# Optimization experiments

Hardware: AMD Instinct MI355X
Metric: run time of the kernel (lower is better)

Reference implementation:

```python
import jax, jax.numpy as jnp
import numpy as np

L_IN, L_FREQ, L_OUT = 128, 64, 64
C_IN, C_OUT, T_DIM = 64, 64, 256
SPIN = 1

# ---------- self-contained spin-weighted SHT (MW sampling), replacing s2fft ----------

def _mw_thetas(L, extended):
    n = 2 * L - 1 if extended else L
    return (2 * np.arange(n) + 1) * np.pi / (2 * L - 1)

def _wigner_d_stack(L, thetas, n):
    # d^l_{m,n}(theta) = <l,m| exp(-i theta Jy) |l,n>, computed via eigh of the
    # Hermitian angular-momentum operator Jy. Output (ntheta, L, 2L-1), m at col L-1+m.
    nth = len(thetas)
    out = np.zeros((nth, L, 2 * L - 1), dtype=np.float64)
    for l in range(abs(n), L):
        dim = 2 * l + 1
        m = np.arange(-l, l).astype(np.float64)
        ap = np.sqrt(l * (l + 1.0) - m * (m + 1.0))
        Jy = np.zeros((dim, dim), dtype=np.complex128)
        i = np.arange(dim - 1)
        Jy[i + 1, i] = -0.5j * ap
        Jy[i, i + 1] = 0.5j * ap
        lam, V = np.linalg.eigh(Jy)
        coeff = V * np.conj(V[l + n, :])[None, :]
        phases = np.exp(-1j * np.outer(lam, thetas))
        out[:, l, L - 1 - l:L + l] = (coeff @ phases).T.real
    return out

def _mw_quad_weights(L):
    # per-theta weights on the mirror-extended grid: q_t = (1/(2L-1)) sum_k w(k) e^{ik theta_t}
    # with w(k) = int_0^pi e^{ik t} sin(t) dt
    k = np.arange(-(L - 1), L)
    den = np.where(np.abs(k) == 1, 1, 1 - k * k).astype(np.float64)
    w = np.where(k % 2 == 0, 2.0 / den, 0.0).astype(np.complex128)
    w[k == 1] = 0.5j * np.pi
    w[k == -1] = -0.5j * np.pi
    th = _mw_thetas(L, True)
    return ((w[None, :] * np.exp(1j * np.outer(th, k))).sum(1) / (2 * L - 1)).real

# transform kernels are constants (built once at import, numpy)
_D_FWD = jnp.asarray(_wigner_d_stack(L_IN, _mw_thetas(L_IN, True), -SPIN) * _mw_quad_weights(L_IN)[:, None, None], jnp.float32)
_D_INV = jnp.asarray(_wigner_d_stack(L_OUT, _mw_thetas(L_OUT, False), -SPIN), jnp.float32)
_CL_IN = jnp.asarray(((-1.0) ** SPIN) * np.sqrt((2 * np.arange(L_IN) + 1) / (4 * np.pi)), jnp.float32)
_CL_OUT = jnp.asarray(((-1.0) ** SPIN) * np.sqrt((2 * np.arange(L_OUT) + 1) / (4 * np.pi)), jnp.float32)
_m_all = np.arange(-(L_IN - 1), L_IN)
_PARITY = jnp.asarray(np.where((_m_all + SPIN) % 2 == 0, 1.0, -1.0), jnp.float32)

def sht_forward(x):
    # x: (L_IN, 2*L_IN-1, C) real spatial -> flm: (L_IN, 2*L_IN-1, C) complex, m at L_IN-1+m
    nphi = 2 * L_IN - 1
    ftm = jnp.fft.fftshift(jnp.fft.fft(x, axis=1), axes=1) * (2 * jnp.pi / nphi)
    # mirror extension in theta with (-1)^(m+spin) parity (all channels at once)
    g_ext = jnp.concatenate([ftm, _PARITY[None, :, None] * ftm[::-1][1:]], axis=0)
    flm = jnp.einsum('tlm,tmc->lmc', _D_FWD, g_ext)
    return flm * _CL_IN[:, None, None]

def sht_inverse(flm):
    # flm: (L_OUT, 2*L_OUT-1, C) complex -> (L_OUT, 2*L_OUT-1, C) real spatial
    ftm = jnp.einsum('tlm,lmc->tmc', _D_INV, flm * _CL_OUT[:, None, None])
    return (jnp.fft.ifft(jnp.fft.ifftshift(ftm, axes=1), axis=1) * (2 * L_OUT - 1)).real

def resize_flm(flm, l_in, l_out):
    # centered truncation / zero-pad of (L, 2L-1, C) harmonic coefficients
    if l_out <= l_in:
        d = l_in - l_out
        return flm[:l_out, d:d + 2 * l_out - 1]
    d = l_out - l_in
    return jnp.pad(flm, ((0, d), (d, d), (0, 0)))

# ---------- inputs and parameters ----------

def setup_inputs():
    key = jax.random.key(0)
    ks = jax.random.split(key, 12)
    n = lambda i, shape, s: jax.random.normal(ks[i], shape, jnp.float32) * s
    return {
        'x': jax.random.normal(ks[0], (L_IN, 2 * L_IN - 1, C_IN), jnp.float32),
        't_emb': jax.random.normal(ks[1], (T_DIM,), jnp.float32),
        'spec_conv_w': n(2, (C_IN, C_OUT), (1.0 / C_IN) ** 0.5),
        'spec_conv_b': jnp.zeros((C_OUT,), jnp.float32),
        'spec_wr': n(3, (L_FREQ, C_IN, C_OUT), (0.5 / C_IN) ** 0.5),
        'spec_wi': n(4, (L_FREQ, C_IN, C_OUT), (0.5 / C_IN) ** 0.5),
        'spec_tr_w': n(5, (T_DIM, L_FREQ), (1.0 / T_DIM) ** 0.5),
        'spec_tr_b': jnp.zeros((L_FREQ,), jnp.float32),
        'spec_ti_w': n(6, (T_DIM, L_FREQ), (1.0 / T_DIM) ** 0.5),
        'spec_ti_b': jnp.zeros((L_FREQ,), jnp.float32),
        'spat_conv1_w': n(7, (C_IN, C_OUT), (1.0 / C_IN) ** 0.5),
        'spat_conv1_b': jnp.zeros((C_OUT,), jnp.float32),
        'spat_t_w': n(8, (T_DIM, 2 * C_OUT), (1.0 / T_DIM) ** 0.5),
        'spat_t_b': jnp.zeros((2 * C_OUT,), jnp.float32),
        'spat_weight': n(9, (C_OUT, C_OUT), 0.01),
        'spat_conv2_w': n(10, (C_OUT, C_OUT), (1.0 / C_OUT) ** 0.5),
        'spat_conv2_b': jnp.zeros((C_OUT,), jnp.float32),
        'ln_scale': jnp.ones((C_OUT,), jnp.float32),
        'ln_bias': jnp.zeros((C_OUT,), jnp.float32),
    }

def reference(x, t_emb, spec_conv_w, spec_conv_b, spec_wr, spec_wi, spec_tr_w, spec_tr_b, spec_ti_w, spec_ti_b, spat_conv1_w, spat_conv1_b, spat_t_w, spat_t_b, spat_weight, spat_conv2_w, spat_conv2_b, ln_scale, ln_bias):
    # ----- SphericalSpectralTimeConv branch -----
    flm = sht_forward(x)                                   # (L_IN, 2L_IN-1, C_IN) complex
    flm = resize_flm(flm, L_IN, L_FREQ)                    # (L_FREQ, 2L_FREQ-1, C_IN)
    conv_flm = jnp.einsum('lmi,io->lmo', flm, spec_conv_w) + spec_conv_b
    t_c = (t_emb @ spec_tr_w + spec_tr_b) + 1j * (t_emb @ spec_ti_w + spec_ti_b)   # (L_FREQ,)
    w = t_c[:, None, None] * (spec_wr + 1j * spec_wi)      # (L_FREQ, C_IN, C_OUT)
    flm = jnp.einsum('lmi,lio->lmo', flm, w) + conv_flm
    xs = sht_inverse(resize_flm(flm, L_FREQ, L_OUT))       # (L_OUT, 2L_OUT-1, C_OUT) real
    xs = xs / (jnp.linalg.norm(xs, axis=-1, keepdims=True) + 1e-6)
    # ----- SpatialTimeConv branch (path='down') -----
    h = jnp.einsum('lmi,io->lmo', x, spat_conv1_w) + spat_conv1_b
    t = t_emb @ spat_t_w + spat_t_b
    w_t, b_t = t[:C_OUT], t[C_OUT:]
    h = jnp.einsum('lmi,io->lmo', h, w_t[None, :] * spat_weight)
    h = sht_inverse(resize_flm(sht_forward(h), L_IN, L_OUT))
    h = jnp.einsum('lmi,io->lmo', h, spat_conv2_w) + spat_conv2_b + b_t
    # ----- combine: add, gelu, LayerNorm (eps=1e-6 over channels) -----
    y = jax.nn.gelu(xs + h)
    mu = jnp.mean(y, axis=-1, keepdims=True)
    var = jnp.var(y, axis=-1, keepdims=True)
    return (y - mu) * jax.lax.rsqrt(var + 1e-6) * ln_scale + ln_bias
```

## Files before the change

### kernel.cpp

```cpp
#include <hip/hip_runtime.h>
#include <math.h>

#define DPI 3.141592653589793238462643383279502884

__device__ __forceinline__ float wave_sum64(float v) {
#pragma unroll
  for (int off = 32; off > 0; off >>= 1) v += __shfl_xor(v, off, 64);
  return v;
}

__device__ __forceinline__ float gelu_tanh(float v) {
  float u = 0.7978845608028654f * (v + 0.044715f * v * v * v);
  return 0.5f * v * (1.0f + tanhf(u));
}

#define CN255F ((float)(-2.0 * DPI / 255.0))
#define CN127F ((float)(2.0 * DPI / 127.0))


__device__ __forceinline__ void dft_block(int idx, int tid, const float* __restrict__ x,
                                          float* __restrict__ Are, float* __restrict__ Aim,
                                          float* __restrict__ Bre, float* __restrict__ Bim,
                                          char* sm) {
  float* xs_ = (float*)sm;
  int t = idx >> 2, ph = (idx >> 1) & 1, mh = idx & 1;
  float* ore = ph ? Bre : Are;
  float* oim = ph ? Bim : Aim;
  int pbase = ph * 128;
  int Ktot = ph ? 127 : 128;
  int cg_ = tid & 15, mg = tid >> 4;
  float wr[2], wi[2], rc[2], rs[2];
#pragma unroll
  for (int j = 0; j < 2; ++j) {
    int m = mh * 32 + mg * 2 + j;
    __sincosf(CN255F * (float)m, &rs[j], &rc[j]);
    int r0 = (m * pbase) % 255;
    __sincosf(CN255F * (float)r0, &wi[j], &wr[j]);
  }
  float accr[2][4], acci[2][4];
#pragma unroll
  for (int j = 0; j < 2; ++j)
#pragma unroll
    for (int q = 0; q < 4; ++q) { accr[j][q] = 0.f; acci[j][q] = 0.f; }
  for (int k0 = 0; k0 < Ktot; k0 += 64) {
    int kn = (Ktot - k0 < 64) ? Ktot - k0 : 64;
    __syncthreads();
    {
      const float4* src = (const float4*)(x + ((size_t)t * 255 + pbase + k0) * 64);
      float4* dst = (float4*)xs_;
      int lim = kn * 16;
#pragma unroll
      for (int q = 0; q < 4; ++q) {
        int fidx = tid + q * 256;
        if (fidx < lim) dst[fidx] = src[fidx];
      }
    }
    __syncthreads();
#pragma unroll 2
    for (int k = 0; k < kn; ++k) {
      float4 xv = *(const float4*)&xs_[k * 64 + cg_ * 4];
      float xv4[4] = {xv.x, xv.y, xv.z, xv.w};
#pragma unroll
      for (int j = 0; j < 2; ++j) {
#pragma unroll
        for (int q = 0; q < 4; ++q) {
          accr[j][q] = fmaf(xv4[q], wr[j], accr[j][q]);
          acci[j][q] = fmaf(xv4[q], wi[j], acci[j][q]);
        }
        float nw = wr[j] * rc[j] - wi[j] * rs[j];
        wi[j] = fmaf(wr[j], rs[j], wi[j] * rc[j]);
        wr[j] = nw;
      }
    }
  }
#pragma unroll
  for (int j = 0; j < 2; ++j) {
    int mi = mh * 32 + mg * 2 + j;
    size_t ob = ((size_t)t * 64 + mi) * 64 + cg_ * 4;
    *(float4*)(ore + ob) = make_float4(accr[j][0], accr[j][1], accr[j][2], accr[j][3]);
    *(float4*)(oim + ob) = make_float4(acci[j][0], acci[j][1], acci[j][2], acci[j][3]);
  }
}

__device__ __forceinline__ void wigner_block(int wb, int tid, float* __restrict__ Deff,
                                             float* __restrict__ Dinv, char* sm) {
  float* LF = (float*)sm;
  double* red = (double*)(sm + 512);
  float* clf = (float*)(sm + 1024);
  int mode = (wb < 128) ? 0 : 1;
  int t, mm;
  if (mode == 0) { t = wb; mm = tid; }
  else { mm = wb - 128; t = (tid < 64) ? tid : 63; }
  if (tid < 64) clf[tid] = (float)(-sqrt((2.0 * tid + 1.0) / (4.0 * DPI)));
  if (tid < 128) LF[tid] = (tid == 0) ? 0.f : logf((float)tid);
  __syncthreads();
  for (int s = 1; s < 128; s <<= 1) {
    float add = (tid < 128 && tid >= s) ? LF[tid - s] : 0.f;
    __syncthreads();
    if (tid < 128) LF[tid] += add;
    __syncthreads();
  }
  double denomN = (mode == 0) ? 255.0 : 127.0;
  double beta = (2.0 * t + 1.0) * DPI / denomN;
  float coeff = 1.0f;
  if (mode == 0) {
    if (tid < 63) {
      int k = 2 * (tid + 1);
      red[tid] = 8.0 * cos((double)k * beta) / (1.0 - (double)k * (double)k);
    } else if (tid == 63) {
      red[63] = 4.0;
    }
    __syncthreads();
    for (int s = 32; s > 0; s >>= 1) {
      if (tid < s) red[tid] += red[tid + s];
      __syncthreads();
    }
    double s = red[0] / 255.0;
    if (t == 127) s *= 0.5;
    coeff = (float)(s * (2.0 * DPI / 255.0));
  }
  bool active = (mode == 0) ? (tid < 127) : (tid < 64);
  if (!active) return;
  int m = mm - 63;
  double chd, shd;
  sincos(0.5 * beta, &shd, &chd);
  float cbf = (float)cos(beta);
  float chf = (float)chd, shf = (float)shd;
  int am = (m < 0) ? -m : m;
  int l0v = (am > 1) ? am : 1;
  float seed;
  if (m == 0) {
    seed = -1.4142135623730951f * shf * chf;
  } else {
    int j = am;
    float lch = logf(chf), lsh = logf(shf);
    float e0 = 0.5f * (LF[2 * j] - LF[j - 1] - LF[j + 1]);
    float expo = (m >= 1) ? e0 + (float)(j - 1) * lch + (float)(j + 1) * lsh
                          : e0 + (float)(j + 1) * lch + (float)(j - 1) * lsh;
    float sv = __expf(expo);
    seed = (m >= 1 && ((m + 1) & 1)) ? -sv : sv;
  }
  float dl = seed, dm1 = 0.0f, S_cur = 0.0f;
  float mf = (float)m;
  for (int l = 0; l < 64; ++l) {
    float val = 0.0f;
    if (l >= l0v) {
      val = dl * coeff * clf[l];
      float Ld = (float)l, lp = Ld + 1.0f;
      float S_next = sqrtf((lp * lp - mf * mf) * (lp * lp - 1.0f));
      float num1 = (2.0f * Ld + 1.0f) * (Ld * lp * cbf + mf);
      float dn = (num1 * dl - lp * S_cur * dm1) / (Ld * S_next);
      dm1 = dl; dl = dn; S_cur = S_next;
    }
    if (mode == 0) Deff[((size_t)t * 127 + mm) * 64 + l] = val;
    else Dinv[((size_t)mm * 64 + l) * 64 + t] = val;
  }
}

__device__ __forceinline__ void a2_block(int l, int tid, const float* __restrict__ temb,
                                         const float* __restrict__ trw, const float* __restrict__ trb,
                                         const float* __restrict__ tiw, const float* __restrict__ tib,
                                         const float* __restrict__ scw, const float* __restrict__ swr,
                                         const float* __restrict__ swi, float2* __restrict__ A2,
                                         char* sm) {
  float* fb1 = (float*)sm;
  float* fb2 = (float*)(sm + 1024);
  fb1[tid] = temb[tid] * trw[tid * 64 + l];
  fb2[tid] = temb[tid] * tiw[tid * 64 + l];
  __syncthreads();
  for (int s = 128; s > 0; s >>= 1) {
    if (tid < s) { fb1[tid] += fb1[tid + s]; fb2[tid] += fb2[tid + s]; }
    __syncthreads();
  }
  float tr = fb1[0] + trb[l], ti = fb2[0] + tib[l];
  int o = tid & 63, iq = tid >> 6;
  for (int i = iq * 16; i < iq * 16 + 16; ++i) {
    int idx = (l * 64 + i) * 64 + o;
    float r = swr[idx], s2 = swi[idx];
    A2[idx] = make_float2(scw[i * 64 + o] + tr * r - ti * s2, tr * s2 + ti * r);
  }
}

__device__ __forceinline__ void m_block(int j, int tid, const float* __restrict__ temb,
                                        const float* __restrict__ stw, const float* __restrict__ stb,
                                        const float* __restrict__ c1w, const float* __restrict__ c1b,
                                        const float* __restrict__ sweight, float* __restrict__ Mm,
                                        float* __restrict__ bias2, char* sm) {
  float* fb1 = (float*)sm;
  float* fb2 = (float*)(sm + 1024);
  int o = tid & 63, part = tid >> 6;
  float p = 0.f;
  for (int k = part * 64; k < part * 64 + 64; ++k)
    p = fmaf(temb[k], stw[k * 128 + o], p);
  fb1[part * 64 + o] = p;
  __syncthreads();
  if (part == 0) fb2[o] = fb1[o] + fb1[64 + o] + fb1[128 + o] + fb1[192 + o] + stb[o];
  __syncthreads();
  float tvo = fb2[o];
  float q = 0.f;
  for (int i = part * 16; i < part * 16 + 16; ++i)
    q = fmaf(c1w[j * 64 + i], sweight[i * 64 + o], q);
  __syncthreads();
  fb1[part * 64 + o] = q;
  __syncthreads();
  if (part == 0) Mm[j * 64 + o] = tvo * (fb1[o] + fb1[64 + o] + fb1[128 + o] + fb1[192 + o]);
  if (j == 0) {
    float bq = 0.f;
    for (int i = part * 16; i < part * 16 + 16; ++i)
      bq = fmaf(c1b[i], sweight[i * 64 + o], bq);
    __syncthreads();
    fb1[part * 64 + o] = bq;
    __syncthreads();
    if (part == 0) bias2[o] = tvo * (fb1[o] + fb1[64 + o] + fb1[128 + o] + fb1[192 + o]);
  }
}

__device__ __forceinline__ void tv_block(int tid, const float* __restrict__ temb,
                                         const float* __restrict__ stw, const float* __restrict__ stb,
                                         float* __restrict__ tv, char* sm) {
  float* fb1 = (float*)sm;
  int o = tid & 127, part = tid >> 7;
  float p = 0.f;
  for (int k = part * 128; k < part * 128 + 128; ++k)
    p = fmaf(temb[k], stw[k * 128 + o], p);
  fb1[part * 128 + o] = p;
  __syncthreads();
  if (part == 0) tv[o] = fb1[o] + fb1[128 + o] + stb[o];
}

__global__ __launch_bounds__(256, 2) void ct_pre(
    const float* __restrict__ x, const float* __restrict__ temb,
    const float* __restrict__ trw, const float* __restrict__ trb,
    const float* __restrict__ tiw, const float* __restrict__ tib,
    const float* __restrict__ stw, const float* __restrict__ stb,
    const float* __restrict__ scw, const float* __restrict__ swr,
    const float* __restrict__ swi, const float* __restrict__ c1w,
    const float* __restrict__ c1b, const float* __restrict__ sweight,
    float* __restrict__ Deff, float* __restrict__ Dinv,
    float2* __restrict__ A2, float* __restrict__ Mm,
    float* __restrict__ bias2, float* __restrict__ tv,
    float* __restrict__ ftmA_re, float* __restrict__ ftmA_im,
    float* __restrict__ ftmB_re, float* __restrict__ ftmB_im) {
  __shared__ __align__(16) char sm[16384];
  int vb = blockIdx.x;
  int tid = threadIdx.x;
  if (vb < 255) wigner_block(vb, tid, Deff, Dinv, sm);
  else if (vb < 319) a2_block(vb - 255, tid, temb, trw, trb, tiw, tib, scw, swr, swi, A2, sm);
  else if (vb < 383) m_block(vb - 319, tid, temb, stw, stb, c1w, c1b, sweight, Mm, bias2, sm);
  else if (vb < 384) tv_block(tid, temb, stw, stb, tv, sm);
  else dft_block(vb - 384, tid, x, ftmA_re, ftmA_im, ftmB_re, ftmB_im, sm);
}

__global__ __launch_bounds__(256) void ct_projf(const float* __restrict__ Deff,
                                                const float* __restrict__ fAre,
                                                const float* __restrict__ fAim,
                                                const float* __restrict__ fBre,
                                                const float* __restrict__ fBim,
                                                float* __restrict__ flmA_re, float* __restrict__ flmA_im,
                                                float* __restrict__ flmB_re, float* __restrict__ flmB_im) {
  __shared__ float Dsh[64][32];
  __shared__ float fr_[64][64], fi_[64][64];
  int mm = blockIdx.x, lh = blockIdx.y, th = blockIdx.z;
  float* ore = th ? flmB_re : flmA_re;
  float* oim = th ? flmB_im : flmA_im;
  int tb = th * 64;
  int mi = (mm >= 63) ? (mm - 63) : (63 - mm);
  float csign = (mm >= 63) ? 1.0f : -1.0f;
  int tid = threadIdx.x;
  int cg_ = tid & 15, lg = tid >> 4;
  for (int e = tid; e < 64 * 32; e += 256) {
    int r = e >> 5, li = e & 31;
    Dsh[r][li] = Deff[((size_t)(tb + r) * 127 + mm) * 64 + lh * 32 + li];
  }
  for (int e = tid; e < 64 * 64; e += 256) {
    int r = e >> 6, c = e & 63;
    size_t idx = ((size_t)(tb + r) * 64 + mi) * 64 + c;
    fr_[r][c] = fAre[idx] + fBre[idx];
    fi_[r][c] = csign * (fAim[idx] + fBim[idx]);
  }
  __syncthreads();
  float ar[2][4], ai[2][4];
#pragma unroll
  for (int li = 0; li < 2; ++li)
#pragma unroll
    for (int q = 0; q < 4; ++q) { ar[li][q] = 0.f; ai[li][q] = 0.f; }
#pragma unroll 4
  for (int k = 0; k < 64; ++k) {
    float4 fr4 = *(const float4*)&fr_[k][cg_ * 4];
    float4 fi4 = *(const float4*)&fi_[k][cg_ * 4];
    float2 d2 = *(const float2*)&Dsh[k][lg * 2];
    float frv[4] = {fr4.x, fr4.y, fr4.z, fr4.w};
    float fiv[4] = {fi4.x, fi4.y, fi4.z, fi4.w};
    float dv[2] = {d2.x, d2.y};
#pragma unroll
    for (int li = 0; li < 2; ++li)
#pragma unroll
      for (int q = 0; q < 4; ++q) {
        ar[li][q] = fmaf(dv[li], frv[q], ar[li][q]);
        ai[li][q] = fmaf(dv[li], fiv[q], ai[li][q]);
      }
  }
#pragma unroll
  for (int li = 0; li < 2; ++li) {
    size_t row = ((size_t)mm * 64 + lh * 32 + lg * 2 + li) * 64 + cg_ * 4;
    *(float4*)(ore + row) = make_float4(ar[li][0], ar[li][1], ar[li][2], ar[li][3]);
    *(float4*)(oim + row) = make_float4(ai[li][0], ai[li][1], ai[li][2], ai[li][3]);
  }
}

__global__ __launch_bounds__(256) void ct_mix(const float* __restrict__ flmA_re,
                                              const float* __restrict__ flmA_im,
                                              const float* __restrict__ flmB_re,
                                              const float* __restrict__ flmB_im,
                                              const float2* __restrict__ A2,
                                              const float* __restrict__ Mm,
                                              const float* __restrict__ scb,
                                              const float* __restrict__ bias2,
                                              const float* __restrict__ Deff,
                                              float* __restrict__ s_re, float* __restrict__ s_im,
                                              float* __restrict__ h_re, float* __restrict__ h_im) {
  __shared__ float Ar_[64][32], Ai_[64][32], Msh[64][32];
  __shared__ float Br_[64][65], Bi_[64][65];
  __shared__ float rb[256];
  int l = blockIdx.x, mh = blockIdx.y, oh = blockIdx.z;
  int tid = threadIdx.x;
  int og = tid & 15, mg = tid >> 4;
  rb[tid] = (mh == 0 && tid < 128) ? Deff[((size_t)tid * 127 + 63) * 64 + l] : 0.f;
  __syncthreads();
  for (int s = 128; s > 0; s >>= 1) {
    if (tid < s) rb[tid] += rb[tid + s];
    __syncthreads();
  }
  float slv = rb[0];
  for (int e = tid; e < 64 * 32; e += 256) {
    int r = e >> 5, oi = e & 31;
    float2 aa = A2[((size_t)l * 64 + r) * 64 + oh * 32 + oi];
    Ar_[r][oi] = aa.x; Ai_[r][oi] = aa.y;
    Msh[r][oi] = Mm[r * 64 + oh * 32 + oi];
  }
  for (int e = tid; e < 64 * 64; e += 256) {
    int mi = e >> 6, i = e & 63;
    int gmm = mh * 64 + mi; if (gmm > 126) gmm = 126;
    size_t idx = ((size_t)gmm * 64 + l) * 64 + i;
    Br_[mi][i] = flmA_re[idx] + flmB_re[idx];
    Bi_[mi][i] = flmA_im[idx] + flmB_im[idx];
  }
  __syncthreads();
  int o0 = oh * 32 + og * 2;
  float b0[2] = {scb[o0], scb[o0 + 1]};
  float sr[4][2], si[4][2], hr[4][2], hi[4][2];
#pragma unroll
  for (int jm = 0; jm < 4; ++jm)
#pragma unroll
    for (int qo = 0; qo < 2; ++qo) {
      sr[jm][qo] = b0[qo]; si[jm][qo] = 0.f; hr[jm][qo] = 0.f; hi[jm][qo] = 0.f;
    }
#pragma unroll 4
  for (int k = 0; k < 64; ++k) {
    float2 ar2 = *(const float2*)&Ar_[k][og * 2];
    float2 ai2 = *(const float2*)&Ai_[k][og * 2];
    float2 mv2 = *(const float2*)&Msh[k][og * 2];
    float br4[4], bi4[4];
#pragma unroll
    for (int jm = 0; jm < 4; ++jm) {
      br4[jm] = Br_[mg * 4 + jm][k];
      bi4[jm] = Bi_[mg * 4 + jm][k];
    }
    float arv[2] = {ar2.x, ar2.y}, aiv[2] = {ai2.x, ai2.y}, mvv[2] = {mv2.x, mv2.y};
#pragma unroll
    for (int jm = 0; jm < 4; ++jm)
#pragma unroll
      for (int qo = 0; qo < 2; ++qo) {
        sr[jm][qo] = fmaf(br4[jm], arv[qo], sr[jm][qo]);
        sr[jm][qo] = fmaf(-bi4[jm], aiv[qo], sr[jm][qo]);
        si[jm][qo] = fmaf(br4[jm], aiv[qo], si[jm][qo]);
        si[jm][qo] = fmaf(bi4[jm], arv[qo], si[jm][qo]);
        hr[jm][qo] = fmaf(br4[jm], mvv[qo], hr[jm][qo]);
        hi[jm][qo] = fmaf(bi4[jm], mvv[qo], hi[jm][qo]);
      }
  }
  float bb[2] = {bias2[o0], bias2[o0 + 1]};
#pragma unroll
  for (int jm = 0; jm < 4; ++jm) {
    int gmm = mh * 64 + mg * 4 + jm;
    if (gmm > 126) continue;
    if (gmm == 63) {
#pragma unroll
      for (int qo = 0; qo < 2; ++qo)
        hr[jm][qo] = fmaf(255.0f * slv, bb[qo], hr[jm][qo]);
    }
    size_t row = ((size_t)gmm * 64 + l) * 64 + o0;
    *(float2*)(s_re + row) = make_float2(sr[jm][0], sr[jm][1]);
    *(float2*)(s_im + row) = make_float2(si[jm][0], si[jm][1]);
    *(float2*)(h_re + row) = make_float2(hr[jm][0], hr[jm][1]);
    *(float2*)(h_im + row) = make_float2(hi[jm][0], hi[jm][1]);
  }
}

__global__ __launch_bounds__(256) void ct_proji(const float* __restrict__ Dinv,
                                                const float* __restrict__ s_re,
                                                const float* __restrict__ s_im,
                                                const float* __restrict__ h_re,
                                                const float* __restrict__ h_im,
                                                float* __restrict__ fos_re, float* __restrict__ fos_im,
                                                float* __restrict__ foh_re, float* __restrict__ foh_im) {
  __shared__ float Dsh[64][64];
  __shared__ float Br_[64][32], Bi_[64][32];
  int mm = blockIdx.x, br = blockIdx.y, ch = blockIdx.z;
  const float* ire = br ? h_re : s_re;
  const float* iim = br ? h_im : s_im;
  float* ore = br ? foh_re : fos_re;
  float* oim = br ? foh_im : fos_im;
  int tid = threadIdx.x;
  int cg_ = tid & 15, tg = tid >> 4;
  for (int e = tid; e < 64 * 64; e += 256) {
    int r = e >> 6, tt = e & 63;
    Dsh[r][tt] = Dinv[((size_t)mm * 64 + r) * 64 + tt];
  }
  for (int e = tid; e < 64 * 32; e += 256) {
    int r = e >> 5, cc = e & 31;
    size_t idx = ((size_t)mm * 64 + r) * 64 + ch * 32 + cc;
    Br_[r][cc] = ire[idx];
    Bi_[r][cc] = iim[idx];
  }
  __syncthreads();
  float ar[4][2], ai[4][2];
#pragma unroll
  for (int j = 0; j < 4; ++j)
#pragma unroll
    for (int q = 0; q < 2; ++q) { ar[j][q] = 0.f; ai[j][q] = 0.f; }
#pragma unroll 4
  for (int k = 0; k < 64; ++k) {
    float4 d4 = *(const float4*)&Dsh[k][tg * 4];
    float2 fr2 = *(const float2*)&Br_[k][cg_ * 2];
    float2 fi2 = *(const float2*)&Bi_[k][cg_ * 2];
    float dv[4] = {d4.x, d4.y, d4.z, d4.w};
    float frv[2] = {fr2.x, fr2.y}, fiv[2] = {fi2.x, fi2.y};
#pragma unroll
    for (int j = 0; j < 4; ++j)
#pragma unroll
      for (int q = 0; q < 2; ++q) {
        ar[j][q] = fmaf(dv[j], frv[q], ar[j][q]);
        ai[j][q] = fmaf(dv[j], fiv[q], ai[j][q]);
      }
  }
#pragma unroll
  for (int j = 0; j < 4; ++j) {
    int t = tg * 4 + j;
    size_t ob = ((size_t)t * 127 + mm) * 64 + ch * 32 + cg_ * 2;
    *(float2*)(ore + ob) = make_float2(ar[j][0], ar[j][1]);
    *(float2*)(oim + ob) = make_float2(ai[j][0], ai[j][1]);
  }
}

__global__ __launch_bounds__(256) void ct_idft(const float* __restrict__ fos_re,
                                               const float* __restrict__ fos_im,
                                               const float* __restrict__ foh_re,
                                               const float* __restrict__ foh_im,
                                               float* __restrict__ xsbA, float* __restrict__ xsbB,
                                               float* __restrict__ hsbA, float* __restrict__ hsbB) {
  __shared__ float Br_[32][64], Bi_[32][64];
  int t = blockIdx.x, br = blockIdx.y;
  int z = blockIdx.z;
  int ph = z >> 1, kh = z & 1;
  const float* fre = br ? foh_re : fos_re;
  const float* fim = br ? foh_im : fos_im;
  float* outp = br ? (kh ? hsbB : hsbA) : (kh ? xsbB : xsbA);
  int kbase = kh * 64;
  int Ktot = kh ? 63 : 64;
  int tid = threadIdx.x;
  int cg_ = tid & 15, pg = tid >> 4;
  float wc[4], ws[4], rc[4], rs[4];
#pragma unroll
  for (int j = 0; j < 4; ++j) {
    int gp = ph * 64 + pg * 4 + j; if (gp > 126) gp = 126;
    __sincosf(CN127F * (float)gp, &rs[j], &rc[j]);
    int r0 = ((kbase - 63) * gp) % 127;
    __sincosf(CN127F * (float)r0, &ws[j], &wc[j]);
  }
  float acc[4][4];
#pragma unroll
  for (int j = 0; j < 4; ++j)
#pragma unroll
    for (int q = 0; q < 4; ++q) acc[j][q] = 0.f;
  for (int k0 = 0; k0 < Ktot; k0 += 32) {
    int kn = (Ktot - k0 < 32) ? Ktot - k0 : 32;
    __syncthreads();
    for (int e = tid; e < 32 * 64; e += 256) {
      int r = e >> 6, j = e & 63;
      if (r < kn) {
        size_t bidx = ((size_t)t * 127 + kbase + k0 + r) * 64 + j;
        Br_[r][j] = fre[bidx]; Bi_[r][j] = fim[bidx];
      }
    }
    __syncthreads();
#pragma unroll 2
    for (int k = 0; k < kn; ++k) {
      float4 b_r = *(const float4*)&Br_[k][cg_ * 4];
      float4 b_i = *(const float4*)&Bi_[k][cg_ * 4];
      float brv[4] = {b_r.x, b_r.y, b_r.z, b_r.w};
      float biv[4] = {b_i.x, b_i.y, b_i.z, b_i.w};
#pragma unroll
      for (int j = 0; j < 4; ++j) {
#pragma unroll
        for (int q = 0; q < 4; ++q) {
          acc[j][q] = fmaf(brv[q], wc[j], acc[j][q]);
          acc[j][q] = fmaf(biv[q], -ws[j], acc[j][q]);
        }
        float nw = wc[j] * rc[j] - ws[j] * rs[j];
        ws[j] = fmaf(wc[j], rs[j], ws[j] * rc[j]);
        wc[j] = nw;
      }
    }
  }
#pragma unroll
  for (int j = 0; j < 4; ++j) {
    int gp = ph * 64 + pg * 4 + j;
    if (gp > 126) continue;
    *(float4*)(outp + ((size_t)t * 127 + gp) * 64 + cg_ * 4) =
        make_float4(acc[j][0], acc[j][1], acc[j][2], acc[j][3]);
  }
}

__global__ __launch_bounds__(256) void ct_fin(const float* __restrict__ xsbA,
                                              const float* __restrict__ xsbB,
                                              const float* __restrict__ hsbA,
                                              const float* __restrict__ hsbB,
                                              const float* __restrict__ c2w,
                                              const float* __restrict__ c2b,
                                              const float* __restrict__ tv,
                                              const float* __restrict__ lns,
                                              const float* __restrict__ lnb,
                                              float* __restrict__ out) {
  int w = threadIdx.x >> 6, lane = threadIdx.x & 63;
  size_t row = (size_t)blockIdx.x * 4 + w;
  size_t base = row * 64 + lane;
  float hv = hsbA[base] + hsbB[base];
  float xv = xsbA[base] + xsbB[base];
  float acc = c2b[lane] + tv[64 + lane];
#pragma unroll 16
  for (int i = 0; i < 64; ++i)
    acc = fmaf(__shfl(hv, i, 64), c2w[i * 64 + lane], acc);
  float ss = wave_sum64(xv * xv);
  xv = xv / (sqrtf(ss) + 1e-6f);
  float y = xv + acc;
  float g = gelu_tanh(y);
  float mu = wave_sum64(g) * (1.0f / 64.0f);
  float d = g - mu;
  float var = wave_sum64(d * d) * (1.0f / 64.0f);
  out[base] = d * rsqrtf(var + 1e-6f) * lns[lane] + lnb[lane];
}

extern "C" void kernel_launch(void* const* d_in, const int* in_sizes, int n_in,
                              void* d_out, int out_size, void* d_ws, size_t ws_size,
                              hipStream_t stream) {
  const float* x = (const float*)d_in[0];
  const float* temb = (const float*)d_in[1];
  const float* scw = (const float*)d_in[2];
  const float* scb = (const float*)d_in[3];
  const float* swr = (const float*)d_in[4];
  const float* swi = (const float*)d_in[5];
  const float* strw = (const float*)d_in[6];
  const float* strb = (const float*)d_in[7];
  const float* stiw = (const float*)d_in[8];
  const float* stib = (const float*)d_in[9];
  const float* c1w = (const float*)d_in[10];
  const float* c1b = (const float*)d_in[11];
  const float* stw = (const float*)d_in[12];
  const float* stb = (const float*)d_in[13];
  const float* sweight = (const float*)d_in[14];
  const float* c2w = (const float*)d_in[15];
  const float* c2b = (const float*)d_in[16];
  const float* lns = (const float*)d_in[17];
  const float* lnb = (const float*)d_in[18];
  float* out = (float*)d_out;

  char* base = (char*)d_ws;
  size_t off = 0;
  auto alloc = [&](size_t bytes) -> void* {
    void* p = base + off;
    off += (bytes + 255) & ~(size_t)255;
    return p;
  };
  float* tv = (float*)alloc(128 * sizeof(float));
  float* Mm = (float*)alloc(4096 * sizeof(float));
  float* bias2 = (float*)alloc(64 * sizeof(float));
  float2* A2 = (float2*)alloc(262144 * sizeof(float2));
  float* Deff = (float*)alloc(1040384 * sizeof(float));
  float* Dinv = (float*)alloc(520192 * sizeof(float));
  float* ftmA_re = (float*)alloc(524288 * sizeof(float));
  float* ftmA_im = (float*)alloc(524288 * sizeof(float));
  float* ftmB_re = (float*)alloc(524288 * sizeof(float));
  float* ftmB_im = (float*)alloc(524288 * sizeof(float));
  float* flmA_re = (float*)alloc(520192 * sizeof(float));
  float* flmA_im = (float*)alloc(520192 * sizeof(float));
  float* flmB_re = (float*)alloc(520192 * sizeof(float));
  float* flmB_im = (float*)alloc(520192 * sizeof(float));
  if (off > ws_size) return;
  float* s_re = ftmA_re;
  float* s_im = ftmA_im;
  float* h_re = ftmB_re;
  float* h_im = ftmB_im;
  float* fos_re = Deff;
  float* fos_im = Deff + 520192;
  float* foh_re = flmA_re;
  float* foh_im = flmA_im;
  float* xsbA = flmB_re;
  float* xsbB = flmB_im;
  float* hsbA = ftmA_re;
  float* hsbB = ftmA_im;

  hipLaunchKernelGGL(ct_pre, dim3(896), dim3(256), 0, stream,
                     x, temb, strw, strb, stiw, stib, stw, stb,
                     scw, swr, swi, c1w, c1b, sweight,
                     Deff, Dinv, A2, Mm, bias2, tv,
                     ftmA_re, ftmA_im, ftmB_re, ftmB_im);
  hipLaunchKernelGGL(ct_projf, dim3(127, 2, 2), dim3(256), 0, stream, Deff,
                     ftmA_re, ftmA_im, ftmB_re, ftmB_im,
                     flmA_re, flmA_im, flmB_re, flmB_im);
  hipLaunchKernelGGL(ct_mix, dim3(64, 2, 2), dim3(256), 0, stream,
                     flmA_re, flmA_im, flmB_re, flmB_im, A2, Mm, scb, bias2, Deff,
                     s_re, s_im, h_re, h_im);
  hipLaunchKernelGGL(ct_proji, dim3(127, 2, 2), dim3(256), 0, stream, Dinv,
                     s_re, s_im, h_re, h_im, fos_re, fos_im, foh_re, foh_im);
  hipLaunchKernelGGL(ct_idft, dim3(64, 2, 4), dim3(256), 0, stream,
                     fos_re, fos_im, foh_re, foh_im, xsbA, xsbB, hsbA, hsbB);
  hipLaunchKernelGGL(ct_fin, dim3(2032), dim3(256), 0, stream, xsbA, xsbB, hsbA, hsbB,
                     c2w, c2b, tv, lns, lnb, out);
}
```

Before: 193.9 us.

## Split precompute and DFT kernels, stage Wigner tables through LDS for coalesced stores

Splits the combined ct_pre launch into a setup kernel (Wigner, A2, M, tv blocks) and a separate DFT kernel, each with its own launch shape and shared-memory size. The forward Wigner table is written through a padded shared buffer in two halves, so stores to Deff become coalesced instead of strided per thread. The recurrence also uses fast sqrt and reciprocal intrinsics. This adds one kernel launch and some barriers, and the fast intrinsics may change precision slightly.

Result: slower. 205.8 us (+6.1%).

```diff
diff --git a/kernel.cpp b/kernel.cpp
--- a/kernel.cpp
+++ b/kernel.cpp
@@ -17,76 +17,13 @@
 #define CN255F ((float)(-2.0 * DPI / 255.0))
 #define CN127F ((float)(2.0 * DPI / 127.0))
 
-
-__device__ __forceinline__ void dft_block(int idx, int tid, const float* __restrict__ x,
-                                          float* __restrict__ Are, float* __restrict__ Aim,
-                                          float* __restrict__ Bre, float* __restrict__ Bim,
-                                          char* sm) {
-  float* xs_ = (float*)sm;
-  int t = idx >> 2, ph = (idx >> 1) & 1, mh = idx & 1;
-  float* ore = ph ? Bre : Are;
-  float* oim = ph ? Bim : Aim;
-  int pbase = ph * 128;
-  int Ktot = ph ? 127 : 128;
-  int cg_ = tid & 15, mg = tid >> 4;
-  float wr[2], wi[2], rc[2], rs[2];
-#pragma unroll
-  for (int j = 0; j < 2; ++j) {
-    int m = mh * 32 + mg * 2 + j;
-    __sincosf(CN255F * (float)m, &rs[j], &rc[j]);
-    int r0 = (m * pbase) % 255;
-    __sincosf(CN255F * (float)r0, &wi[j], &wr[j]);
-  }
-  float accr[2][4], acci[2][4];
-#pragma unroll
-  for (int j = 0; j < 2; ++j)
-#pragma unroll
-    for (int q = 0; q < 4; ++q) { accr[j][q] = 0.f; acci[j][q] = 0.f; }
-  for (int k0 = 0; k0 < Ktot; k0 += 64) {
-    int kn = (Ktot - k0 < 64) ? Ktot - k0 : 64;
-    __syncthreads();
-    {
-      const float4* src = (const float4*)(x + ((size_t)t * 255 + pbase + k0) * 64);
-      float4* dst = (float4*)xs_;
-      int lim = kn * 16;
-#pragma unroll
-      for (int q = 0; q < 4; ++q) {
-        int fidx = tid + q * 256;
-        if (fidx < lim) dst[fidx] = src[fidx];
-      }
-    }
-    __syncthreads();
-#pragma unroll 2
-    for (int k = 0; k < kn; ++k) {
-      float4 xv = *(const float4*)&xs_[k * 64 + cg_ * 4];
-      float xv4[4] = {xv.x, xv.y, xv.z, xv.w};
-#pragma unroll
-      for (int j = 0; j < 2; ++j) {
-#pragma unroll
-        for (int q = 0; q < 4; ++q) {
-          accr[j][q] = fmaf(xv4[q], wr[j], accr[j][q]);
-          acci[j][q] = fmaf(xv4[q], wi[j], acci[j][q]);
-        }
-        float nw = wr[j] * rc[j] - wi[j] * rs[j];
-        wi[j] = fmaf(wr[j], rs[j], wi[j] * rc[j]);
-        wr[j] = nw;
-      }
-    }
-  }
-#pragma unroll
-  for (int j = 0; j < 2; ++j) {
-    int mi = mh * 32 + mg * 2 + j;
-    size_t ob = ((size_t)t * 64 + mi) * 64 + cg_ * 4;
-    *(float4*)(ore + ob) = make_float4(accr[j][0], accr[j][1], accr[j][2], accr[j][3]);
-    *(float4*)(oim + ob) = make_float4(acci[j][0], acci[j][1], acci[j][2], acci[j][3]);
-  }
-}
 
 __device__ __forceinline__ void wigner_block(int wb, int tid, float* __restrict__ Deff,
                                              float* __restrict__ Dinv, char* sm) {
   float* LF = (float*)sm;
   double* red = (double*)(sm + 512);
   float* clf = (float*)(sm + 1024);
+  float* smD = (float*)(sm + 1280);
   int mode = (wb < 128) ? 0 : 1;
   int t, mm;
   if (mode == 0) { t = wb; mm = tid; }
@@ -120,40 +57,68 @@
     coeff = (float)(s * (2.0 * DPI / 255.0));
   }
   bool active = (mode == 0) ? (tid < 127) : (tid < 64);
-  if (!active) return;
   int m = mm - 63;
-  double chd, shd;
-  sincos(0.5 * beta, &shd, &chd);
-  float cbf = (float)cos(beta);
-  float chf = (float)chd, shf = (float)shd;
   int am = (m < 0) ? -m : m;
   int l0v = (am > 1) ? am : 1;
-  float seed;
-  if (m == 0) {
-    seed = -1.4142135623730951f * shf * chf;
-  } else {
-    int j = am;
-    float lch = logf(chf), lsh = logf(shf);
-    float e0 = 0.5f * (LF[2 * j] - LF[j - 1] - LF[j + 1]);
-    float expo = (m >= 1) ? e0 + (float)(j - 1) * lch + (float)(j + 1) * lsh
-                          : e0 + (float)(j + 1) * lch + (float)(j - 1) * lsh;
-    float sv = __expf(expo);
-    seed = (m >= 1 && ((m + 1) & 1)) ? -sv : sv;
-  }
-  float dl = seed, dm1 = 0.0f, S_cur = 0.0f;
+  float dl = 0.f, dm1 = 0.f, S_cur = 0.f, cbf = 0.f;
   float mf = (float)m;
-  for (int l = 0; l < 64; ++l) {
-    float val = 0.0f;
-    if (l >= l0v) {
-      val = dl * coeff * clf[l];
-      float Ld = (float)l, lp = Ld + 1.0f;
-      float S_next = sqrtf((lp * lp - mf * mf) * (lp * lp - 1.0f));
-      float num1 = (2.0f * Ld + 1.0f) * (Ld * lp * cbf + mf);
-      float dn = (num1 * dl - lp * S_cur * dm1) / (Ld * S_next);
-      dm1 = dl; dl = dn; S_cur = S_next;
-    }
-    if (mode == 0) Deff[((size_t)t * 127 + mm) * 64 + l] = val;
-    else Dinv[((size_t)mm * 64 + l) * 64 + t] = val;
+  if (active) {
+    double chd, shd;
+    sincos(0.5 * beta, &shd, &chd);
+    cbf = (float)cos(beta);
+    float chf = (float)chd, shf = (float)shd;
+    float seed;
+    if (m == 0) {
+      seed = -1.4142135623730951f * shf * chf;
+    } else {
+      int j = am;
+      float lch = logf(chf), lsh = logf(shf);
+      float e0 = 0.5f * (LF[2 * j] - LF[j - 1] - LF[j + 1]);
+      float expo = (m >= 1) ? e0 + (float)(j - 1) * lch + (float)(j + 1) * lsh
+                            : e0 + (float)(j + 1) * lch + (float)(j - 1) * lsh;
+      float sv = __expf(expo);
+      seed = (m >= 1 && ((m + 1) & 1)) ? -sv : sv;
+    }
+    dl = seed;
+  }
+  if (mode == 1) {
+    if (!active) return;
+    for (int l = 0; l < 64; ++l) {
+      float val = 0.0f;
+      if (l >= l0v) {
+        val = dl * coeff * clf[l];
+        float Ld = (float)l, lp = Ld + 1.0f;
+        float S_next = __fsqrt_rn((lp * lp - mf * mf) * (lp * lp - 1.0f));
+        float num1 = (2.0f * Ld + 1.0f) * (Ld * lp * cbf + mf);
+        float dn = (num1 * dl - lp * S_cur * dm1) * __fdividef(1.0f, Ld * S_next);
+        dm1 = dl; dl = dn; S_cur = S_next;
+      }
+      Dinv[((size_t)mm * 64 + l) * 64 + t] = val;
+    }
+    return;
+  }
+  for (int half = 0; half < 2; ++half) {
+    if (active) {
+      for (int li = 0; li < 32; ++li) {
+        int l = half * 32 + li;
+        float val = 0.0f;
+        if (l >= l0v) {
+          val = dl * coeff * clf[l];
+          float Ld = (float)l, lp = Ld + 1.0f;
+          float S_next = __fsqrt_rn((lp * lp - mf * mf) * (lp * lp - 1.0f));
+          float num1 = (2.0f * Ld + 1.0f) * (Ld * lp * cbf + mf);
+          float dn = (num1 * dl - lp * S_cur * dm1) * __fdividef(1.0f, Ld * S_next);
+          dm1 = dl; dl = dn; S_cur = S_next;
+        }
+        smD[mm * 33 + li] = val;
+      }
+    }
+    __syncthreads();
+    for (int e = tid; e < 127 * 32; e += 256) {
+      int mmw = e >> 5, li = e & 31;
+      Deff[((size_t)t * 127 + mmw) * 64 + half * 32 + li] = smD[mmw * 33 + li];
+    }
+    __syncthreads();
   }
 }
 
@@ -228,8 +193,8 @@
   if (part == 0) tv[o] = fb1[o] + fb1[128 + o] + stb[o];
 }
 
-__global__ __launch_bounds__(256, 2) void ct_pre(
-    const float* __restrict__ x, const float* __restrict__ temb,
+__global__ __launch_bounds__(256) void ct_setup(
+    const float* __restrict__ temb,
     const float* __restrict__ trw, const float* __restrict__ trb,
     const float* __restrict__ tiw, const float* __restrict__ tib,
     const float* __restrict__ stw, const float* __restrict__ stb,
@@ -238,17 +203,79 @@
     const float* __restrict__ c1b, const float* __restrict__ sweight,
     float* __restrict__ Deff, float* __restrict__ Dinv,
     float2* __restrict__ A2, float* __restrict__ Mm,
-    float* __restrict__ bias2, float* __restrict__ tv,
-    float* __restrict__ ftmA_re, float* __restrict__ ftmA_im,
-    float* __restrict__ ftmB_re, float* __restrict__ ftmB_im) {
-  __shared__ __align__(16) char sm[16384];
+    float* __restrict__ bias2, float* __restrict__ tv) {
+  __shared__ __align__(16) char sm[18176];
   int vb = blockIdx.x;
   int tid = threadIdx.x;
   if (vb < 255) wigner_block(vb, tid, Deff, Dinv, sm);
   else if (vb < 319) a2_block(vb - 255, tid, temb, trw, trb, tiw, tib, scw, swr, swi, A2, sm);
   else if (vb < 383) m_block(vb - 319, tid, temb, stw, stb, c1w, c1b, sweight, Mm, bias2, sm);
-  else if (vb < 384) tv_block(tid, temb, stw, stb, tv, sm);
-  else dft_block(vb - 384, tid, x, ftmA_re, ftmA_im, ftmB_re, ftmB_im, sm);
+  else tv_block(tid, temb, stw, stb, tv, sm);
+}
+
+__global__ __launch_bounds__(256) void ct_dft(const float* __restrict__ x,
+                                              float* __restrict__ Are, float* __restrict__ Aim,
+                                              float* __restrict__ Bre, float* __restrict__ Bim) {
+  __shared__ __align__(16) float xs_[64 * 64];
+  int idx = blockIdx.x;
+  int tid = threadIdx.x;
+  int t = idx >> 2, ph = (idx >> 1) & 1, mh = idx & 1;
+  float* ore = ph ? Bre : Are;
+  float* oim = ph ? Bim : Aim;
+  int pbase = ph * 128;
+  int Ktot = ph ? 127 : 128;
+  int cg_ = tid & 15, mg = tid >> 4;
+  float wr[2], wi[2], rc[2], rs[2];
+#pragma unroll
+  for (int j = 0; j < 2; ++j) {
+    int m = mh * 32 + mg * 2 + j;
+    __sincosf(CN255F * (float)m, &rs[j], &rc[j]);
+    int r0 = (m * pbase) % 255;
+    __sincosf(CN255F * (float)r0, &wi[j], &wr[j]);
+  }
+  float accr[2][4], acci[2][4];
+#pragma unroll
+  for (int j = 0; j < 2; ++j)
+#pragma unroll
+    for (int q = 0; q < 4; ++q) { accr[j][q] = 0.f; acci[j][q] = 0.f; }
+  for (int k0 = 0; k0 < Ktot; k0 += 64) {
+    int kn = (Ktot - k0 < 64) ? Ktot - k0 : 64;
+    __syncthreads();
+    {
+      const float4* src = (const float4*)(x + ((size_t)t * 255 + pbase + k0) * 64);
+      float4* dst = (float4*)xs_;
+      int lim = kn * 16;
+#pragma unroll
+      for (int q = 0; q < 4; ++q) {
+        int fidx = tid + q * 256;
+        if (fidx < lim) dst[fidx] = src[fidx];
+      }
+    }
+    __syncthreads();
+#pragma unroll 2
+    for (int k = 0; k < kn; ++k) {
+      float4 xv = *(const float4*)&xs_[k * 64 + cg_ * 4];
+      float xv4[4] = {xv.x, xv.y, xv.z, xv.w};
+#pragma unroll
+      for (int j = 0; j < 2; ++j) {
+#pragma unroll
+        for (int q = 0; q < 4; ++q) {
+          accr[j][q] = fmaf(xv4[q], wr[j], accr[j][q]);
+          acci[j][q] = fmaf(xv4[q], wi[j], acci[j][q]);
+        }
+        float nw = wr[j] * rc[j] - wi[j] * rs[j];
+        wi[j] = fmaf(wr[j], rs[j], wi[j] * rc[j]);
+        wr[j] = nw;
+      }
+    }
+  }
+#pragma unroll
+  for (int j = 0; j < 2; ++j) {
+    int mi = mh * 32 + mg * 2 + j;
+    size_t ob = ((size_t)t * 64 + mi) * 64 + cg_ * 4;
+    *(float4*)(ore + ob) = make_float4(accr[j][0], accr[j][1], accr[j][2], accr[j][3]);
+    *(float4*)(oim + ob) = make_float4(acci[j][0], acci[j][1], acci[j][2], acci[j][3]);
+  }
 }
 
 __global__ __launch_bounds__(256) void ct_projf(const float* __restrict__ Deff,
@@ -610,11 +637,12 @@
   float* hsbA = ftmA_re;
   float* hsbB = ftmA_im;
 
-  hipLaunchKernelGGL(ct_pre, dim3(896), dim3(256), 0, stream,
-                     x, temb, strw, strb, stiw, stib, stw, stb,
+  hipLaunchKernelGGL(ct_setup, dim3(384), dim3(256), 0, stream,
+                     temb, strw, strb, stiw, stib, stw, stb,
                      scw, swr, swi, c1w, c1b, sweight,
-                     Deff, Dinv, A2, Mm, bias2, tv,
-                     ftmA_re, ftmA_im, ftmB_re, ftmB_im);
+                     Deff, Dinv, A2, Mm, bias2, tv);
+  hipLaunchKernelGGL(ct_dft, dim3(512), dim3(256), 0, stream,
+                     x, ftmA_re, ftmA_im, ftmB_re, ftmB_im);
   hipLaunchKernelGGL(ct_projf, dim3(127, 2, 2), dim3(256), 0, stream, Deff,
                      ftmA_re, ftmA_im, ftmB_re, ftmB_im,
                      flmA_re, flmA_im, flmB_re, flmB_im);
```
